# Kernel tuning notes

Hardware: AMD Instinct MI355X
Metric: run time of the kernel (lower is better)

## Reference

```python
import jax, jax.numpy as jnp
import numpy as np

ORDER = 7
ALPHA = 1.0
BETA = 1.0

def _jacobi_coeffs(order, a, b):
    k1 = np.zeros(order + 1, dtype=np.float32)
    k2 = np.zeros(order + 1, dtype=np.float32)
    k3 = np.zeros(order + 1, dtype=np.float32)
    for i in range(2, order + 1):
        k1[i] = (2*i + a + b) * (2*i + a + b - 1) / (2*i * (i + a + b))
        k2[i] = (2*i + a + b - 1) * (a*a - b*b) / (2*i * (i + a + b) * (2*i + a + b - 2))
        k3[i] = (i + a - 1) * (i + b - 1) * (2*i + a + b) / (i * (i + a + b) * (2*i + a + b - 2))
    return k1, k2, k3

K1, K2, K3 = _jacobi_coeffs(ORDER, ALPHA, BETA)

def setup_inputs() -> dict:
    key = jax.random.key(0)
    kx, kc = jax.random.split(key)
    batch, input_size, output_size = 4096, 512, 512
    x = jax.random.normal(kx, (batch, input_size), dtype=jnp.float32)
    coef = jax.random.normal(kc, (output_size, input_size, ORDER + 1), dtype=jnp.float32) * 0.1
    return {"x": x, "coef": coef}

def _precompute_jacobi(x):
    # x: [B, I] -> jacobi values [B, I, order+1]
    x = jnp.tanh(x)
    p0 = jnp.ones_like(x)
    p1 = 0.5 * (ALPHA + BETA + 2.0) * x - 0.5 * (ALPHA - BETA)
    vals = [p0, p1]
    for i in range(2, ORDER + 1):
        vals.append((K1[i] * x + K2[i]) * vals[i - 1] - K3[i] * vals[i - 2])
    return jnp.stack(vals, axis=2)  # [B, I, D]

def reference(x, coef):
    jac = _precompute_jacobi(x)                 # [B, I, D]
    # sum_j over input and order dims in one contraction
    return jnp.einsum('bid,jid->bj', jac, coef)  # [B, O]
```

## Files before the change

kernel.cpp:

```cpp
#include <hip/hip_runtime.h>
#include <stdint.h>

#define BATCH 4096
#define ISZ   512
#define OSZ   512
#define KDIM  4096

#define TM 128
#define TN 128
#define BK 64
#define SPLITK 8

typedef __bf16 bf16x8 __attribute__((ext_vector_type(8)));
typedef float  f32x4  __attribute__((ext_vector_type(4)));

__device__ __forceinline__ unsigned short f2bf(float f) {
    uint32_t u = __float_as_uint(f);
    u = (u + 0x7FFFu + ((u >> 16) & 1u)) >> 16;
    return (unsigned short)u;
}

__global__ __launch_bounds__(256) void convert_bf16(
    const float* __restrict__ src, unsigned short* __restrict__ dst, int n4)
{
    int idx = blockIdx.x * 256 + threadIdx.x;
    if (idx >= n4) return;
    float4 v = reinterpret_cast<const float4*>(src)[idx];
    uint2 o;
    o.x = (uint32_t)f2bf(v.x) | ((uint32_t)f2bf(v.y) << 16);
    o.y = (uint32_t)f2bf(v.z) | ((uint32_t)f2bf(v.w) << 16);
    reinterpret_cast<uint2*>(dst)[idx] = o;
}

__global__ __launch_bounds__(256) void gemm_fused(
    const float* __restrict__ X,
    const unsigned short* __restrict__ Bm,
    unsigned short* __restrict__ Cp,
    int M, int N, int K)
{
    __shared__ __align__(16) unsigned short As[TM * BK];
    __shared__ __align__(16) unsigned short Bs[TN * BK];

    const int tid  = threadIdx.x;
    const int wave = tid >> 6;
    const int lane = tid & 63;
    const int wm   = (wave >> 1) * 64;
    const int wn   = (wave & 1) * 64;

    const int    m0    = blockIdx.x * TM;
    const size_t baseB = (size_t)blockIdx.y * TN * K;
    const int kper  = K / SPLITK;
    const int kbeg  = blockIdx.z * kper;
    const int kend  = kbeg + kper;

    f32x4 acc[4][4] = {};

    const int mrow = lane & 15;
    const int kc   = lane >> 4;

    const int xr = tid >> 1;
    const int xc = (tid & 1) * 4;

    for (int k0 = kbeg; k0 < kend; k0 += BK) {
        #pragma unroll
        for (int it = 0; it < 4; ++it) {
            int s    = it * 256 + tid;
            int row  = s >> 3;
            int csrc = (s & 7) ^ (row & 7);
            const unsigned short* gB = Bm + baseB + (size_t)row * K + k0 + csrc * 8;
            unsigned short* lB = Bs + (size_t)(it * 256 + wave * 64) * 8;
            __builtin_amdgcn_global_load_lds(
                (const __attribute__((address_space(1))) uint32_t*)gB,
                (__attribute__((address_space(3))) uint32_t*)lB, 16, 0, 0);
        }

        {
            const int i0 = k0 >> 3;
            float4 xv = *reinterpret_cast<const float4*>(
                X + (size_t)(m0 + xr) * ISZ + i0 + xc);
            const float xs[4] = {xv.x, xv.y, xv.z, xv.w};
            #pragma unroll
            for (int j = 0; j < 4; ++j) {
                float e  = __expf(2.0f * xs[j]);
                float t  = 1.0f - 2.0f * __builtin_amdgcn_rcpf(e + 1.0f);
                float p1 = 2.0f * t;
                float p2 = (1.875f     * t) * p1 - 0.75f;
                float p3 = (1.8666667f * t) * p2 - 0.8f        * p1;
                float p4 = (1.875f     * t) * p3 - 0.83333333f * p2;
                float p5 = (1.8857143f * t) * p4 - 0.85714287f * p3;
                float p6 = (1.8958333f * t) * p5 - 0.875f      * p4;
                float p7 = (1.9047619f * t) * p6 - 0.88888889f * p5;
                bf16x8 v;
                v[0] = (__bf16)1.0f; v[1] = (__bf16)p1;
                v[2] = (__bf16)p2;   v[3] = (__bf16)p3;
                v[4] = (__bf16)p4;   v[5] = (__bf16)p5;
                v[6] = (__bf16)p6;   v[7] = (__bf16)p7;
                int slot = xr * 8 + ((xc + j) ^ (xr & 7));
                *reinterpret_cast<bf16x8*>(As + (size_t)slot * 8) = v;
            }
        }
        __syncthreads();

        #pragma unroll
        for (int ks = 0; ks < BK; ks += 32) {
            bf16x8 aF[4], bF[4];
            const int cbase = (ks >> 3) + kc;
            #pragma unroll
            for (int mi = 0; mi < 4; ++mi) {
                int r = wm + mi * 16 + mrow;
                int slot = r * 8 + (cbase ^ (r & 7));
                aF[mi] = *reinterpret_cast<const bf16x8*>(As + (size_t)slot * 8);
            }
            #pragma unroll
            for (int ni = 0; ni < 4; ++ni) {
                int r = wn + ni * 16 + mrow;
                int slot = r * 8 + (cbase ^ (r & 7));
                bF[ni] = *reinterpret_cast<const bf16x8*>(Bs + (size_t)slot * 8);
            }
            #pragma unroll
            for (int mi = 0; mi < 4; ++mi)
                #pragma unroll
                for (int ni = 0; ni < 4; ++ni)
                    acc[mi][ni] = __builtin_amdgcn_mfma_f32_16x16x32_bf16(
                        aF[mi], bF[ni], acc[mi][ni], 0, 0, 0);
        }
        __syncthreads();
    }

    unsigned short* Cz = Cp + (size_t)blockIdx.z * M * N;
    const int orow = blockIdx.x * TM + wm + (lane >> 4) * 4;
    const int ocol = blockIdx.y * TN + wn + (lane & 15);
    #pragma unroll
    for (int mi = 0; mi < 4; ++mi)
        #pragma unroll
        for (int ni = 0; ni < 4; ++ni)
            #pragma unroll
            for (int r = 0; r < 4; ++r)
                Cz[(size_t)(orow + mi * 16 + r) * N + ocol + ni * 16] =
                    f2bf(acc[mi][ni][r]);
}

__global__ __launch_bounds__(256) void reduce_k(
    const unsigned short* __restrict__ part, float* __restrict__ out, int n4)
{
    int idx = blockIdx.x * 256 + threadIdx.x;
    if (idx >= n4) return;
    const uint2* p = reinterpret_cast<const uint2*>(part);
    float s0 = 0.f, s1 = 0.f, s2 = 0.f, s3 = 0.f;
    #pragma unroll
    for (int z = 0; z < SPLITK; ++z) {
        uint2 v = p[(size_t)z * n4 + idx];
        s0 += __uint_as_float((v.x & 0xFFFFu) << 16);
        s1 += __uint_as_float(v.x & 0xFFFF0000u);
        s2 += __uint_as_float((v.y & 0xFFFFu) << 16);
        s3 += __uint_as_float(v.y & 0xFFFF0000u);
    }
    float4 o = {s0, s1, s2, s3};
    reinterpret_cast<float4*>(out)[idx] = o;
}

extern "C" void kernel_launch(void* const* d_in, const int* in_sizes, int n_in,
                              void* d_out, int out_size, void* d_ws, size_t ws_size,
                              hipStream_t stream)
{
    const float* x    = (const float*)d_in[0];
    const float* coef = (const float*)d_in[1];
    float* out = (float*)d_out;

    unsigned short* part  = (unsigned short*)d_ws;
    unsigned short* coefb = part + (size_t)SPLITK * BATCH * OSZ;

    int n4c = (OSZ * KDIM) / 4;
    convert_bf16<<<(n4c + 255) / 256, 256, 0, stream>>>(coef, coefb, n4c);

    dim3 grid(BATCH / TM, OSZ / TN, SPLITK);
    gemm_fused<<<grid, 256, 0, stream>>>(x, coefb, part, BATCH, OSZ, KDIM);

    int n4r = (BATCH * OSZ) / 4;
    reduce_k<<<(n4r + 255) / 256, 256, 0, stream>>>(part, out, n4r);
}
```

Measured before the change: 103.1 us.

## Precompute Jacobi bf16 matrix in prep kernel and DMA both GEMM operands

Moves the tanh and Jacobi polynomial expansion out of the GEMM main loop into a combined prep kernel that also converts coef to bf16. This writes a full bf16 A matrix (B x I*8) to workspace. The GEMM then loads both A and B tiles through global_load_lds instead of recomputing the polynomials per block per k-tile. Split-K is halved from 8 to 4, which shrinks the partial buffer and reduction traffic but lowers grid parallelism. The cost is an extra 32 MB write and read of the expanded A matrix.

```diff
diff --git a/kernel.cpp b/kernel.cpp
--- a/kernel.cpp
+++ b/kernel.cpp
@@ -9,7 +9,7 @@
 #define TM 128
 #define TN 128
 #define BK 64
-#define SPLITK 8
+#define SPLITK 4
 
 typedef __bf16 bf16x8 __attribute__((ext_vector_type(8)));
 typedef float  f32x4  __attribute__((ext_vector_type(4)));
@@ -20,20 +20,41 @@
     return (unsigned short)u;
 }
 
-__global__ __launch_bounds__(256) void convert_bf16(
-    const float* __restrict__ src, unsigned short* __restrict__ dst, int n4)
+#define NJAC ((BATCH * ISZ) / 256)
+#define NCVT ((OSZ * KDIM) / 4 / 256)
+__global__ __launch_bounds__(256) void prep(
+    const float* __restrict__ x, unsigned short* __restrict__ jac,
+    const float* __restrict__ coef, unsigned short* __restrict__ coefb)
 {
-    int idx = blockIdx.x * 256 + threadIdx.x;
-    if (idx >= n4) return;
-    float4 v = reinterpret_cast<const float4*>(src)[idx];
-    uint2 o;
-    o.x = (uint32_t)f2bf(v.x) | ((uint32_t)f2bf(v.y) << 16);
-    o.y = (uint32_t)f2bf(v.z) | ((uint32_t)f2bf(v.w) << 16);
-    reinterpret_cast<uint2*>(dst)[idx] = o;
+    int bid = blockIdx.x;
+    if (bid < NJAC) {
+        int idx = bid * 256 + threadIdx.x;
+        float t  = tanhf(x[idx]);
+        float p1 = 2.0f * t;
+        float p2 = (1.875f     * t) * p1 - 0.75f;
+        float p3 = (1.8666667f * t) * p2 - 0.8f        * p1;
+        float p4 = (1.875f     * t) * p3 - 0.83333333f * p2;
+        float p5 = (1.8857143f * t) * p4 - 0.85714287f * p3;
+        float p6 = (1.8958333f * t) * p5 - 0.875f      * p4;
+        float p7 = (1.9047619f * t) * p6 - 0.88888889f * p5;
+        uint4 o;
+        o.x = 0x3F80u | ((uint32_t)f2bf(p1) << 16);
+        o.y = (uint32_t)f2bf(p2) | ((uint32_t)f2bf(p3) << 16);
+        o.z = (uint32_t)f2bf(p4) | ((uint32_t)f2bf(p5) << 16);
+        o.w = (uint32_t)f2bf(p6) | ((uint32_t)f2bf(p7) << 16);
+        *reinterpret_cast<uint4*>(jac + (size_t)idx * 8) = o;
+    } else {
+        int idx = (bid - NJAC) * 256 + threadIdx.x;
+        float4 v = reinterpret_cast<const float4*>(coef)[idx];
+        uint2 o;
+        o.x = (uint32_t)f2bf(v.x) | ((uint32_t)f2bf(v.y) << 16);
+        o.y = (uint32_t)f2bf(v.z) | ((uint32_t)f2bf(v.w) << 16);
+        reinterpret_cast<uint2*>(coefb)[idx] = o;
+    }
 }
 
-__global__ __launch_bounds__(256) void gemm_fused(
-    const float* __restrict__ X,
+__global__ __launch_bounds__(256) void gemm_dma(
+    const unsigned short* __restrict__ A,
     const unsigned short* __restrict__ Bm,
     unsigned short* __restrict__ Cp,
     int M, int N, int K)
@@ -47,19 +68,16 @@
     const int wm   = (wave >> 1) * 64;
     const int wn   = (wave & 1) * 64;
 
-    const int    m0    = blockIdx.x * TM;
+    const size_t baseA = (size_t)blockIdx.x * TM * K;
     const size_t baseB = (size_t)blockIdx.y * TN * K;
-    const int kper  = K / SPLITK;
-    const int kbeg  = blockIdx.z * kper;
-    const int kend  = kbeg + kper;
+    const int kper = K / SPLITK;
+    const int kbeg = blockIdx.z * kper;
+    const int kend = kbeg + kper;
 
     f32x4 acc[4][4] = {};
 
     const int mrow = lane & 15;
     const int kc   = lane >> 4;
-
-    const int xr = tid >> 1;
-    const int xc = (tid & 1) * 4;
 
     for (int k0 = kbeg; k0 < kend; k0 += BK) {
         #pragma unroll
@@ -67,37 +85,16 @@
             int s    = it * 256 + tid;
             int row  = s >> 3;
             int csrc = (s & 7) ^ (row & 7);
+            const unsigned short* gA = A  + baseA + (size_t)row * K + k0 + csrc * 8;
             const unsigned short* gB = Bm + baseB + (size_t)row * K + k0 + csrc * 8;
+            unsigned short* lA = As + (size_t)(it * 256 + wave * 64) * 8;
             unsigned short* lB = Bs + (size_t)(it * 256 + wave * 64) * 8;
+            __builtin_amdgcn_global_load_lds(
+                (const __attribute__((address_space(1))) uint32_t*)gA,
+                (__attribute__((address_space(3))) uint32_t*)lA, 16, 0, 0);
             __builtin_amdgcn_global_load_lds(
                 (const __attribute__((address_space(1))) uint32_t*)gB,
                 (__attribute__((address_space(3))) uint32_t*)lB, 16, 0, 0);
-        }
-
-        {
-            const int i0 = k0 >> 3;
-            float4 xv = *reinterpret_cast<const float4*>(
-                X + (size_t)(m0 + xr) * ISZ + i0 + xc);
-            const float xs[4] = {xv.x, xv.y, xv.z, xv.w};
-            #pragma unroll
-            for (int j = 0; j < 4; ++j) {
-                float e  = __expf(2.0f * xs[j]);
-                float t  = 1.0f - 2.0f * __builtin_amdgcn_rcpf(e + 1.0f);
-                float p1 = 2.0f * t;
-                float p2 = (1.875f     * t) * p1 - 0.75f;
-                float p3 = (1.8666667f * t) * p2 - 0.8f        * p1;
-                float p4 = (1.875f     * t) * p3 - 0.83333333f * p2;
-                float p5 = (1.8857143f * t) * p4 - 0.85714287f * p3;
-                float p6 = (1.8958333f * t) * p5 - 0.875f      * p4;
-                float p7 = (1.9047619f * t) * p6 - 0.88888889f * p5;
-                bf16x8 v;
-                v[0] = (__bf16)1.0f; v[1] = (__bf16)p1;
-                v[2] = (__bf16)p2;   v[3] = (__bf16)p3;
-                v[4] = (__bf16)p4;   v[5] = (__bf16)p5;
-                v[6] = (__bf16)p6;   v[7] = (__bf16)p7;
-                int slot = xr * 8 + ((xc + j) ^ (xr & 7));
-                *reinterpret_cast<bf16x8*>(As + (size_t)slot * 8) = v;
-            }
         }
         __syncthreads();
 
@@ -169,12 +166,12 @@
 
     unsigned short* part  = (unsigned short*)d_ws;
     unsigned short* coefb = part + (size_t)SPLITK * BATCH * OSZ;
+    unsigned short* jac   = coefb + (size_t)OSZ * KDIM;
 
-    int n4c = (OSZ * KDIM) / 4;
-    convert_bf16<<<(n4c + 255) / 256, 256, 0, stream>>>(coef, coefb, n4c);
+    prep<<<NJAC + NCVT, 256, 0, stream>>>(x, jac, coef, coefb);
 
     dim3 grid(BATCH / TM, OSZ / TN, SPLITK);
-    gemm_fused<<<grid, 256, 0, stream>>>(x, coefb, part, BATCH, OSZ, KDIM);
+    gemm_dma<<<grid, 256, 0, stream>>>(jac, coefb, part, BATCH, OSZ, KDIM);
 
     int n4r = (BATCH * OSZ) / 4;
     reduce_k<<<(n4r + 255) / 256, 256, 0, stream>>>(part, out, n4r);
```

Measured after the change: 102.2 us. Within noise of the previous version (-0.9%).
